# Kernel tuning notes

Hardware: AMD Instinct MI355X
Metric: run time of the kernel (lower is better)

The kernel has to match this reference:

```python
import jax, jax.numpy as jnp
import numpy as np

BLOCK_SIZE = 64
HIDDEN = 1024
INTERMEDIATE = 4096
NUM_BLOCK = HIDDEN // BLOCK_SIZE              # 16
INT_BLOCK = (INTERMEDIATE // HIDDEN) * BLOCK_SIZE  # 256


def setup_inputs() -> dict:
    key = jax.random.key(0)
    k_x, k_w1, k_b1, k_w2, k_b2 = jax.random.split(key, 5)
    hidden_states = jax.random.normal(k_x, (4, 2048, HIDDEN), dtype=jnp.float32)
    w1 = 0.02 * jax.random.normal(k_w1, (NUM_BLOCK, INT_BLOCK, BLOCK_SIZE), dtype=jnp.float32)
    b1 = 0.001 * jax.random.normal(k_b1, (INTERMEDIATE,), dtype=jnp.float32)
    w2 = 0.02 * jax.random.normal(k_w2, (NUM_BLOCK, BLOCK_SIZE, INT_BLOCK), dtype=jnp.float32)
    b2 = 0.001 * jax.random.normal(k_b2, (HIDDEN,), dtype=jnp.float32)
    return {"hidden_states": hidden_states, "w1": w1, "b1": b1, "w2": w2, "b2": b2}


def reference(hidden_states, w1, b1, w2, b2):
    lead = hidden_states.shape[:-1]
    dim = hidden_states.shape[-1]
    nb, ibs, bs = w1.shape  # num_block, intermediate_block_size, block_size
    x = hidden_states.reshape(-1, nb, bs)                 # [B, n, i]
    h = jnp.einsum('bni,noi->bno', x, w1)                 # [B, n, o]
    # channel shuffle: transpose block and feature axes before flattening
    h = jnp.swapaxes(h, -1, -2).reshape(-1, nb * ibs)     # [B, o*n order]
    h = jax.nn.gelu(h + b1, approximate=False)
    h = h.reshape(-1, nb, ibs)                            # regroup after shuffle
    y = jnp.einsum('bni,noi->bno', h, w2).reshape(-1, nb * bs) + b2
    return y.reshape(*lead, dim)
```

## Files before the change

kernel.cpp:

```cpp
#include <hip/hip_runtime.h>
#include <hip/hip_bf16.h>


typedef __attribute__((ext_vector_type(8))) short  short8;
typedef __attribute__((ext_vector_type(4))) short  short4v;
typedef __attribute__((ext_vector_type(4))) float  floatx4;

#define XP 1032

__device__ __forceinline__ short f2bf(float f) {
  union { __hip_bfloat16 h; short s; } u;
  u.h = __float2bfloat16(f);
  return u.s;
}
__device__ __forceinline__ float bf2f(short s) {
  union { float f; unsigned u; } uu;
  uu.u = ((unsigned)(unsigned short)s) << 16;
  return uu.f;
}
__device__ __forceinline__ int pk16(float a, float b) {
  return (int)(unsigned short)f2bf(a) | ((int)(unsigned short)f2bf(b) << 16);
}

__device__ __forceinline__ float gelu_f(float v) {
  float m = v * v;
  float c = fmaf(-0.1029375f, m, -2.3020807f);
  float z = v * c;
  float e = __builtin_amdgcn_exp2f(z);
  return v * __builtin_amdgcn_rcpf(1.0f + e);
}

__global__ void pack_k(const float* __restrict__ w1, const float* __restrict__ w2,
                       const float* __restrict__ b1, short* __restrict__ w1p,
                       short* __restrict__ w2p, short* __restrict__ b1p) {
  const int t = blockIdx.x * blockDim.x + threadIdx.x;
  const int lane = t & 63;
  const int lhi = lane >> 4;
  if (t < 32768) {
    const int ks = (t >> 6) & 1, np = (t >> 7) & 15, n = (t >> 11) & 15;
    const float* src = w1 + ((size_t)(n * 256 + np * 16 + (lane & 15)) * 64 + ks * 32 + lhi * 8);
    short8 f;
#pragma unroll
    for (int e = 0; e < 8; ++e) f[e] = f2bf(src[e]);
    *(short8*)(w1p + (size_t)t * 8) = f;
  } else if (t < 65536) {
    const int t2 = t - 32768;
    const int ot = (t2 >> 6) & 3, s = (t2 >> 8) & 7, np = (t2 >> 11) & 15;
    const int op = ot * 16 + (lane & 15);
    short8 f;
#pragma unroll
    for (int e = 0; e < 8; ++e) {
      const int Kc = 32 * s + 16 * ((e >> 2) & 1) + 4 * lhi + (e & 3);
      const int n = Kc >> 4, ohi = Kc & 15;
      f[e] = f2bf(w2[(size_t)(np * 64 + op) * 256 + ohi * 16 + n]);
    }
    *(short8*)(w2p + (size_t)t2 * 8) = f;
  } else {
    const int t3 = t - 65536;
    const int np = (t3 >> 6) & 15, n = (t3 >> 10) & 15;
    short4v b;
#pragma unroll
    for (int r = 0; r < 4; ++r) b[r] = f2bf(b1[(np * 16 + lhi * 4 + r) * 16 + n]);
    *(short4v*)(b1p + (size_t)((n * 16 + np) * 64 + lane) * 4) = b;
  }
}

__global__ __launch_bounds__(256, 4) void pack_x(
    const float* __restrict__ x, short* __restrict__ xT) {
  __shared__ __align__(16) short xs[16 * XP];
  const int tid = threadIdx.x;
  const int wv = tid >> 6, lane = tid & 63;
  const int l15 = lane & 15, lhi = lane >> 4;
  const int rt = blockIdx.x;

#pragma unroll
  for (int j = 0; j < 16; ++j) {
    floatx4 v = __builtin_nontemporal_load(
        (const floatx4*)(x + (size_t)(rt * 16 + j) * 1024 + tid * 4));
    short4v s;
#pragma unroll
    for (int e = 0; e < 4; ++e) s[e] = f2bf(v[e]);
    *(short4v*)(&xs[j * XP + tid * 4]) = s;
  }
  __syncthreads();

#pragma unroll
  for (int i = 0; i < 8; ++i) {
    const int f = wv * 8 + i, n = f >> 1, ks = f & 1;
    short8 fr = *(const short8*)(&xs[l15 * XP + n * 64 + ks * 32 + lhi * 8]);
    *(short8*)(xT + ((size_t)(rt * 16 + n) * 2 + ks) * 512 + lane * 8) = fr;
  }
}

#define XLOAD(P0, P1, P2, P3, ss) {                                            \
  const int n0_ = 2 * (ss), n1_ = n0_ + 1;                                     \
  P0 = *(const short8*)(xT + ((size_t)(rt * 16 + n0_) * 2 + 0) * 512 + lane * 8); \
  P1 = *(const short8*)(xT + ((size_t)(rt * 16 + n0_) * 2 + 1) * 512 + lane * 8); \
  P2 = *(const short8*)(xT + ((size_t)(rt * 16 + n1_) * 2 + 0) * 512 + lane * 8); \
  P3 = *(const short8*)(xT + ((size_t)(rt * 16 + n1_) * 2 + 1) * 512 + lane * 8); \
}

__global__ __launch_bounds__(512, 4) void fused_k(
    const short* __restrict__ xT, const short* __restrict__ w1p,
    const short* __restrict__ w2p, const short* __restrict__ b1p,
    const float* __restrict__ b2, float* __restrict__ y) {
  __shared__ __align__(16) short lw1[16384];
  __shared__ __align__(16) short lw2[16384];
  __shared__ __align__(16) short lb1[4096];

  const int tid = threadIdx.x;
  const int wv = tid >> 6, lane = tid & 63;
  const int l15 = lane & 15, lhi = lane >> 4;
  const int np = blockIdx.x >> 6;
  const int g  = blockIdx.x & 63;
  const int rt = wv * 64 + g;

#pragma unroll
  for (int i = 0; i < 4; ++i) {
    const int u = i * 512 + tid;
    const int c = u >> 6, e = u & 63;
    const size_t so = (((size_t)(c >> 1) * 16 + np) * 2 + (c & 1)) * 512 + e * 8;
    *(short8*)(&lw1[c * 512 + e * 8]) = *(const short8*)(w1p + so);
  }
  {
    const short* src = w2p + (size_t)np * 16384;
#pragma unroll
    for (int i = 0; i < 4; ++i) {
      const int off = (i * 512 + tid) * 8;
      *(short8*)(&lw2[off]) = *(const short8*)(src + off);
    }
  }
  {
    const int n = tid >> 5, e = tid & 31;
    *(short8*)(&lb1[n * 256 + e * 8]) =
        *(const short8*)(b1p + (size_t)(n * 16 + np) * 256 + e * 8);
  }
  __syncthreads();

  floatx4 c0 = {0.f,0.f,0.f,0.f}, c1 = {0.f,0.f,0.f,0.f};
  floatx4 c2 = {0.f,0.f,0.f,0.f}, c3 = {0.f,0.f,0.f,0.f};

  short8 xA0, xA1, xA2, xA3, xB0, xB1, xB2, xB3;
  XLOAD(xA0, xA1, xA2, xA3, 0)

#pragma unroll
  for (int s = 0; s < 8; ++s) {
    if (s < 7) {
      if (s & 1) { XLOAD(xA0, xA1, xA2, xA3, s + 1) }
      else       { XLOAD(xB0, xB1, xB2, xB3, s + 1) }
    }
    const short8 xf00 = (s & 1) ? xB0 : xA0;
    const short8 xf01 = (s & 1) ? xB1 : xA1;
    const short8 xf10 = (s & 1) ? xB2 : xA2;
    const short8 xf11 = (s & 1) ? xB3 : xA3;

    union { int i[4]; short8 v; } af;
    {
      const int n = 2 * s;
      short8 wf0 = *(const short8*)(&lw1[(n * 2 + 0) * 512 + lane * 8]);
      short8 wf1 = *(const short8*)(&lw1[(n * 2 + 1) * 512 + lane * 8]);
      short4v bv = *(const short4v*)(&lb1[n * 256 + lane * 4]);
      floatx4 acc = {0.f, 0.f, 0.f, 0.f};
      acc = __builtin_amdgcn_mfma_f32_16x16x32_bf16(wf0, xf00, acc, 0, 0, 0);
      acc = __builtin_amdgcn_mfma_f32_16x16x32_bf16(wf1, xf01, acc, 0, 0, 0);
      af.i[0] = pk16(gelu_f(acc[0] + bf2f(bv[0])), gelu_f(acc[1] + bf2f(bv[1])));
      af.i[1] = pk16(gelu_f(acc[2] + bf2f(bv[2])), gelu_f(acc[3] + bf2f(bv[3])));
    }
    {
      const int n = 2 * s + 1;
      short8 wf0 = *(const short8*)(&lw1[(n * 2 + 0) * 512 + lane * 8]);
      short8 wf1 = *(const short8*)(&lw1[(n * 2 + 1) * 512 + lane * 8]);
      short4v bv = *(const short4v*)(&lb1[n * 256 + lane * 4]);
      floatx4 acc = {0.f, 0.f, 0.f, 0.f};
      acc = __builtin_amdgcn_mfma_f32_16x16x32_bf16(wf0, xf10, acc, 0, 0, 0);
      acc = __builtin_amdgcn_mfma_f32_16x16x32_bf16(wf1, xf11, acc, 0, 0, 0);
      af.i[2] = pk16(gelu_f(acc[0] + bf2f(bv[0])), gelu_f(acc[1] + bf2f(bv[1])));
      af.i[3] = pk16(gelu_f(acc[2] + bf2f(bv[2])), gelu_f(acc[3] + bf2f(bv[3])));
    }

    short8 bf0  = *(const short8*)(&lw2[(s * 4 + 0) * 512 + lane * 8]);
    short8 bf1  = *(const short8*)(&lw2[(s * 4 + 1) * 512 + lane * 8]);
    short8 bf2v = *(const short8*)(&lw2[(s * 4 + 2) * 512 + lane * 8]);
    short8 bf3  = *(const short8*)(&lw2[(s * 4 + 3) * 512 + lane * 8]);
    c0 = __builtin_amdgcn_mfma_f32_16x16x32_bf16(af.v, bf0,  c0, 0, 0, 0);
    c1 = __builtin_amdgcn_mfma_f32_16x16x32_bf16(af.v, bf1,  c1, 0, 0, 0);
    c2 = __builtin_amdgcn_mfma_f32_16x16x32_bf16(af.v, bf2v, c2, 0, 0, 0);
    c3 = __builtin_amdgcn_mfma_f32_16x16x32_bf16(af.v, bf3,  c3, 0, 0, 0);
  }

  floatx4 cc[4] = {c0, c1, c2, c3};
#pragma unroll
  for (int ot = 0; ot < 4; ++ot) {
    const int col = np * 64 + ot * 16 + l15;
    const float bb = b2[col];
    float* py = y + (size_t)(rt * 16 + lhi * 4) * 1024 + col;
#pragma unroll
    for (int r = 0; r < 4; ++r)
      __builtin_nontemporal_store(cc[ot][r] + bb, py + (size_t)r * 1024);
  }
}

extern "C" void kernel_launch(void* const* d_in, const int* in_sizes, int n_in,
                              void* d_out, int out_size, void* d_ws, size_t ws_size,
                              hipStream_t stream) {
  const float* x  = (const float*)d_in[0];
  const float* w1 = (const float*)d_in[1];
  const float* b1 = (const float*)d_in[2];
  const float* w2 = (const float*)d_in[3];
  const float* b2 = (const float*)d_in[4];
  float* y = (float*)d_out;

  short* w1p = (short*)d_ws;
  short* w2p = w1p + 16 * 256 * 64;
  short* b1p = w2p + 16 * 256 * 64;
  short* xT  = b1p + 16 * 16 * 64 * 4;

  pack_k<<<160, 512, 0, stream>>>(w1, w2, b1, w1p, w2p, b1p);
  pack_x<<<512, 256, 0, stream>>>(x, xT);
  fused_k<<<1024, 512, 0, stream>>>(xT, w1p, w2p, b1p, b2, y);
}
```

Measured before the change: 42.20 us.

## Merge pairs of column-block workgroups into 1024-thread blocks with remapped grid

Doubles the workgroup to 1024 threads so each block covers two adjacent output column blocks, staging both weight slices in shared memory, and halves the grid. The block index is remapped so neighbouring blocks share row groups, which may improve L2 reuse of the packed activations. The trade-off is more LDS per block (about 144KB) and one resident block per CU, which cuts occupancy and the overlap between weight staging and compute across blocks.

```diff
diff --git a/kernel.cpp b/kernel.cpp
--- a/kernel.cpp
+++ b/kernel.cpp
@@ -100,42 +100,54 @@
   P3 = *(const short8*)(xT + ((size_t)(rt * 16 + n1_) * 2 + 1) * 512 + lane * 8); \
 }
 
-__global__ __launch_bounds__(512, 4) void fused_k(
+__global__ __launch_bounds__(1024, 1) void fused_k(
     const short* __restrict__ xT, const short* __restrict__ w1p,
     const short* __restrict__ w2p, const short* __restrict__ b1p,
     const float* __restrict__ b2, float* __restrict__ y) {
-  __shared__ __align__(16) short lw1[16384];
-  __shared__ __align__(16) short lw2[16384];
-  __shared__ __align__(16) short lb1[4096];
+  __shared__ __align__(16) short lw1[2 * 16384];
+  __shared__ __align__(16) short lw2[2 * 16384];
+  __shared__ __align__(16) short lb1[2 * 4096];
 
   const int tid = threadIdx.x;
   const int wv = tid >> 6, lane = tid & 63;
   const int l15 = lane & 15, lhi = lane >> 4;
-  const int np = blockIdx.x >> 6;
-  const int g  = blockIdx.x & 63;
-  const int rt = wv * 64 + g;
+  const int x_  = blockIdx.x & 7;
+  const int pr  = (blockIdx.x >> 3) & 7;
+  const int ghi = blockIdx.x >> 6;
+  const int g   = ghi * 8 + x_;
+  const int npi = wv >> 3;
+  const int np  = pr * 2 + npi;
+  const int rt  = (wv & 7) * 64 + g;
 
 #pragma unroll
   for (int i = 0; i < 4; ++i) {
-    const int u = i * 512 + tid;
-    const int c = u >> 6, e = u & 63;
-    const size_t so = (((size_t)(c >> 1) * 16 + np) * 2 + (c & 1)) * 512 + e * 8;
-    *(short8*)(&lw1[c * 512 + e * 8]) = *(const short8*)(w1p + so);
+    const int u = i * 1024 + tid;
+    const int sl = u >> 11, v = u & 2047;
+    const int c = v >> 6, e = v & 63;
+    const int np_s = pr * 2 + sl;
+    const size_t so = (((size_t)(c >> 1) * 16 + np_s) * 2 + (c & 1)) * 512 + e * 8;
+    *(short8*)(&lw1[sl * 16384 + c * 512 + e * 8]) = *(const short8*)(w1p + so);
+  }
+#pragma unroll
+  for (int i = 0; i < 4; ++i) {
+    const int u = i * 1024 + tid;
+    const int sl = u >> 11, v = u & 2047;
+    const int np_s = pr * 2 + sl;
+    *(short8*)(&lw2[sl * 16384 + v * 8]) =
+        *(const short8*)(w2p + (size_t)np_s * 16384 + v * 8);
   }
   {
-    const short* src = w2p + (size_t)np * 16384;
-#pragma unroll
-    for (int i = 0; i < 4; ++i) {
-      const int off = (i * 512 + tid) * 8;
-      *(short8*)(&lw2[off]) = *(const short8*)(src + off);
-    }
-  }
-  {
-    const int n = tid >> 5, e = tid & 31;
-    *(short8*)(&lb1[n * 256 + e * 8]) =
-        *(const short8*)(b1p + (size_t)(n * 16 + np) * 256 + e * 8);
+    const int sl = tid >> 9, v = tid & 511;
+    const int n = v >> 5, e = v & 31;
+    const int np_s = pr * 2 + sl;
+    *(short8*)(&lb1[sl * 4096 + n * 256 + e * 8]) =
+        *(const short8*)(b1p + (size_t)(n * 16 + np_s) * 256 + e * 8);
   }
   __syncthreads();
+
+  const short* W1 = lw1 + npi * 16384;
+  const short* W2 = lw2 + npi * 16384;
+  const short* B1 = lb1 + npi * 4096;
 
   floatx4 c0 = {0.f,0.f,0.f,0.f}, c1 = {0.f,0.f,0.f,0.f};
   floatx4 c2 = {0.f,0.f,0.f,0.f}, c3 = {0.f,0.f,0.f,0.f};
@@ -157,9 +169,9 @@
     union { int i[4]; short8 v; } af;
     {
       const int n = 2 * s;
-      short8 wf0 = *(const short8*)(&lw1[(n * 2 + 0) * 512 + lane * 8]);
-      short8 wf1 = *(const short8*)(&lw1[(n * 2 + 1) * 512 + lane * 8]);
-      short4v bv = *(const short4v*)(&lb1[n * 256 + lane * 4]);
+      short8 wf0 = *(const short8*)(&W1[(n * 2 + 0) * 512 + lane * 8]);
+      short8 wf1 = *(const short8*)(&W1[(n * 2 + 1) * 512 + lane * 8]);
+      short4v bv = *(const short4v*)(&B1[n * 256 + lane * 4]);
       floatx4 acc = {0.f, 0.f, 0.f, 0.f};
       acc = __builtin_amdgcn_mfma_f32_16x16x32_bf16(wf0, xf00, acc, 0, 0, 0);
       acc = __builtin_amdgcn_mfma_f32_16x16x32_bf16(wf1, xf01, acc, 0, 0, 0);
@@ -168,9 +180,9 @@
     }
     {
       const int n = 2 * s + 1;
-      short8 wf0 = *(const short8*)(&lw1[(n * 2 + 0) * 512 + lane * 8]);
-      short8 wf1 = *(const short8*)(&lw1[(n * 2 + 1) * 512 + lane * 8]);
-      short4v bv = *(const short4v*)(&lb1[n * 256 + lane * 4]);
+      short8 wf0 = *(const short8*)(&W1[(n * 2 + 0) * 512 + lane * 8]);
+      short8 wf1 = *(const short8*)(&W1[(n * 2 + 1) * 512 + lane * 8]);
+      short4v bv = *(const short4v*)(&B1[n * 256 + lane * 4]);
       floatx4 acc = {0.f, 0.f, 0.f, 0.f};
       acc = __builtin_amdgcn_mfma_f32_16x16x32_bf16(wf0, xf10, acc, 0, 0, 0);
       acc = __builtin_amdgcn_mfma_f32_16x16x32_bf16(wf1, xf11, acc, 0, 0, 0);
@@ -178,10 +190,10 @@
       af.i[3] = pk16(gelu_f(acc[2] + bf2f(bv[2])), gelu_f(acc[3] + bf2f(bv[3])));
     }
 
-    short8 bf0  = *(const short8*)(&lw2[(s * 4 + 0) * 512 + lane * 8]);
-    short8 bf1  = *(const short8*)(&lw2[(s * 4 + 1) * 512 + lane * 8]);
-    short8 bf2v = *(const short8*)(&lw2[(s * 4 + 2) * 512 + lane * 8]);
-    short8 bf3  = *(const short8*)(&lw2[(s * 4 + 3) * 512 + lane * 8]);
+    short8 bf0  = *(const short8*)(&W2[(s * 4 + 0) * 512 + lane * 8]);
+    short8 bf1  = *(const short8*)(&W2[(s * 4 + 1) * 512 + lane * 8]);
+    short8 bf2v = *(const short8*)(&W2[(s * 4 + 2) * 512 + lane * 8]);
+    short8 bf3  = *(const short8*)(&W2[(s * 4 + 3) * 512 + lane * 8]);
     c0 = __builtin_amdgcn_mfma_f32_16x16x32_bf16(af.v, bf0,  c0, 0, 0, 0);
     c1 = __builtin_amdgcn_mfma_f32_16x16x32_bf16(af.v, bf1,  c1, 0, 0, 0);
     c2 = __builtin_amdgcn_mfma_f32_16x16x32_bf16(af.v, bf2v, c2, 0, 0, 0);
@@ -217,5 +229,5 @@
 
   pack_k<<<160, 512, 0, stream>>>(w1, w2, b1, w1p, w2p, b1p);
   pack_x<<<512, 256, 0, stream>>>(x, xT);
-  fused_k<<<1024, 512, 0, stream>>>(xT, w1p, w2p, b1p, b2, y);
-}
+  fused_k<<<512, 1024, 0, stream>>>(xT, w1p, w2p, b1p, b2, y);
+}
```

Result: slower. 43.65 us (+3.4%).
